# Kernel tuning notes

Hardware: AMD Instinct MI355X
Metric: run time of the kernel (lower is better)

## Reference

```python
import jax, jax.numpy as jnp
import numpy as np

D_MODEL, D_STATE, D_CONV, EXPAND = 1024, 16, 4, 2
D_INNER = D_MODEL * EXPAND
B, T = 1, 2048
EPS = 1e-5


def setup_inputs() -> dict:
    key = jax.random.key(0)
    ks = jax.random.split(key, 8)
    x = jax.random.normal(ks[0], (B, T, D_MODEL), dtype=jnp.float32)
    W_in = jax.random.normal(ks[1], (D_MODEL, 2 * D_INNER), dtype=jnp.float32) * 0.02
    conv_w = jax.random.normal(ks[2], (D_INNER, D_CONV), dtype=jnp.float32) * 0.2
    conv_b = jax.random.normal(ks[3], (D_INNER,), dtype=jnp.float32) * 0.02
    W_x = jax.random.normal(ks[4], (D_INNER, 2 * D_STATE + 1), dtype=jnp.float32) * 0.02
    W_dt = jax.random.normal(ks[5], (1, D_INNER), dtype=jnp.float32) * 0.5
    b_dt = jax.random.uniform(ks[6], (D_INNER,), dtype=jnp.float32, minval=-0.001, maxval=0.001)
    A_log = jnp.broadcast_to(jnp.log(jnp.arange(1, D_STATE + 1, dtype=jnp.float32))[None, :], (D_INNER, D_STATE))
    Dparam = jnp.ones((D_INNER,), dtype=jnp.float32)
    W_out = jax.random.normal(ks[7], (D_INNER, D_MODEL), dtype=jnp.float32) * 0.02
    ln_g = jnp.ones((D_MODEL,), dtype=jnp.float32)
    ln_b = jnp.zeros((D_MODEL,), dtype=jnp.float32)
    return {"x": x, "W_in": W_in, "conv_w": conv_w, "conv_b": conv_b, "W_x": W_x,
            "W_dt": W_dt, "b_dt": b_dt, "A_log": A_log, "D": Dparam,
            "W_out": W_out, "ln_g": ln_g, "ln_b": ln_b}


def _silu(v):
    return v * jax.nn.sigmoid(v)


def _layernorm(v, g, b):
    mu = jnp.mean(v, axis=-1, keepdims=True)
    var = jnp.mean((v - mu) ** 2, axis=-1, keepdims=True)
    return (v - mu) * jax.lax.rsqrt(var + EPS) * g + b


def _causal_depthwise_conv(xp, conv_w, conv_b):
    # xp: (B, T, D_INNER) -> (B, D_INNER, T) with left pad of D_CONV-1
    xc = jnp.swapaxes(xp, 1, 2)
    xc = jnp.pad(xc, ((0, 0), (0, 0), (D_CONV - 1, 0)))
    w = conv_w[:, None, :]  # (O=D_INNER, I/groups=1, K)
    out = jax.lax.conv_general_dilated(
        xc, w, window_strides=(1,), padding='VALID',
        dimension_numbers=('NCH', 'OIH', 'NCH'), feature_group_count=D_INNER)
    return jnp.swapaxes(out + conv_b[None, :, None], 1, 2)  # (B, T, D_INNER)


def reference(x, W_in, conv_w, conv_b, W_x, W_dt, b_dt, A_log, D, W_out, ln_g, ln_b):
    residual = x
    xn = _layernorm(x, ln_g, ln_b)
    xz = xn @ W_in                      # (B, T, 2*D_INNER)
    x_proj, z = jnp.split(xz, 2, axis=-1)
    x_conv = _silu(_causal_depthwise_conv(x_proj, conv_w, conv_b))  # (B, T, D_INNER)

    ssm = x_conv @ W_x                  # (B, T, 1 + 2*D_STATE)
    dt_raw = ssm[..., :1]
    Bp = ssm[..., 1:1 + D_STATE]        # (B, T, D_STATE)
    Cp = ssm[..., 1 + D_STATE:]         # (B, T, D_STATE)
    dt = jax.nn.softplus(dt_raw @ W_dt + b_dt)  # (B, T, D_INNER)

    A = -jnp.exp(A_log)                 # (D_INNER, D_STATE)
    A_bar = jnp.exp(dt[..., None] * A)                              # (B,T,d,n)
    Bx = dt[..., None] * Bp[:, :, None, :] * x_conv[..., None]      # (B,T,d,n)

    def step(h, inp):
        Ab_t, Bx_t, C_t = inp           # (B,d,n),(B,d,n),(B,n)
        h = Ab_t * h + Bx_t
        y_t = jnp.einsum('bdn,bn->bd', h, C_t)
        return h, y_t

    h0 = jnp.zeros((x.shape[0], D_INNER, D_STATE), dtype=x.dtype)
    _, ys = jax.lax.scan(step, h0, (jnp.swapaxes(A_bar, 0, 1),
                                    jnp.swapaxes(Bx, 0, 1),
                                    jnp.swapaxes(Cp, 0, 1)))
    y = jnp.swapaxes(ys, 0, 1)          # (B, T, D_INNER)

    y = y + x_conv * D
    y = y * _silu(z)
    return y @ W_out + residual
```

## Files before the change

kernel.cpp:

```cpp
#include <hip/hip_runtime.h>
#include <hip/hip_bf16.h>

typedef __hip_bfloat16 bf16;
typedef __attribute__((ext_vector_type(8))) short bf16x8;
typedef __attribute__((ext_vector_type(4))) float f32x4;
typedef __attribute__((ext_vector_type(2))) float f32x2;

#define T_LEN 2048
#define DMODEL 1024
#define DINNER 2048
#define DSTATE 16
#define LN_EPS 1e-5f
#define NCHUNK 128
#define CLEN 16
#define SSTR 64
#define PSEG 131072

#define GLOBAL_AS __attribute__((address_space(1)))
#define LDS_AS __attribute__((address_space(3)))

__device__ __forceinline__ void g2l16(void* lds, const void* g) {
    __builtin_amdgcn_global_load_lds((const GLOBAL_AS void*)g, (LDS_AS void*)lds, 16, 0, 0);
}

__device__ __forceinline__ float b2f(short s) {
    return __uint_as_float(((unsigned)(unsigned short)s) << 16);
}

__device__ __forceinline__ unsigned short f2bu(float f) {
    bf16 b = __float2bfloat16(f);
    return *reinterpret_cast<unsigned short*>(&b);
}

#define BG(buf, j) (buf[(j) >> 2][(j) & 3])

__global__ void prep_all(const float* __restrict__ Win, const float* __restrict__ Wout,
                         const float* __restrict__ Wx, const float* __restrict__ x,
                         const float* __restrict__ lng, const float* __restrict__ lnb,
                         bf16* __restrict__ WinT, bf16* __restrict__ WoutT,
                         bf16* __restrict__ WxT, bf16* __restrict__ xn) {
    __shared__ float t[32][33];
    int bid = blockIdx.x, tid = threadIdx.x;
    int tx = tid & 31, ty4 = (tid >> 5) * 4;
    if (bid < 4096) {
        int n0 = (bid & 127) * 32, k0 = (bid >> 7) * 32;
#pragma unroll
        for (int r = 0; r < 4; r++)
            t[ty4 + r][tx] = Win[(size_t)(k0 + ty4 + r) * 4096 + n0 + tx];
        __syncthreads();
#pragma unroll
        for (int r = 0; r < 4; r++)
            WinT[(size_t)(n0 + ty4 + r) * 1024 + k0 + tx] = __float2bfloat16(t[tx][ty4 + r]);
    } else if (bid < 6144) {
        int b = bid - 4096;
        int n0 = (b & 31) * 32, k0 = (b >> 5) * 32;
#pragma unroll
        for (int r = 0; r < 4; r++)
            t[ty4 + r][tx] = Wout[(size_t)(k0 + ty4 + r) * 1024 + n0 + tx];
        __syncthreads();
#pragma unroll
        for (int r = 0; r < 4; r++)
            WoutT[(size_t)(n0 + ty4 + r) * 2048 + k0 + tx] = __float2bfloat16(t[tx][ty4 + r]);
    } else if (bid < 6656) {
        int idx = (bid - 6144) * 256 + tid;
        int n = idx >> 11, k = idx & 2047;
        int j = (n == 0) ? 0 : (n >= 4 && n <= 35) ? n - 3 : -1;
        WxT[idx] = __float2bfloat16(j >= 0 ? Wx[k * 33 + j] : 0.f);
    } else {
        int row = bid - 6656;
        const float* xr = x + (size_t)row * DMODEL;
        float v[4];
        float s = 0.f, q = 0.f;
#pragma unroll
        for (int i = 0; i < 4; i++) {
            v[i] = xr[tid + i * 256];
            s += v[i];
            q += v[i] * v[i];
        }
        __shared__ float sh_s[256], sh_q[256];
        sh_s[tid] = s; sh_q[tid] = q;
        __syncthreads();
        for (int st = 128; st > 0; st >>= 1) {
            if (tid < st) { sh_s[tid] += sh_s[tid + st]; sh_q[tid] += sh_q[tid + st]; }
            __syncthreads();
        }
        float mean = sh_s[0] * (1.f / DMODEL);
        float var  = sh_q[0] * (1.f / DMODEL) - mean * mean;
        float rstd = rsqrtf(var + LN_EPS);
#pragma unroll
        for (int i = 0; i < 4; i++) {
            int c = tid + i * 256;
            xn[(size_t)row * DMODEL + c] =
                __float2bfloat16((v[i] - mean) * rstd * lng[c] + lnb[c]);
        }
    }
}

template <int BM, int BN, int WAVE_M, int WAVE_N, int WRITE_RESID, int OUT_BF16>
__global__ void gemm_mfma(const bf16* __restrict__ A, const bf16* __restrict__ Bt,
                          void* __restrict__ Cv, const float* __restrict__ resid,
                          int M, int N, int Kslice, int lda) {
    constexpr int WMsz = BM / WAVE_M;
    constexpr int WNsz = BN / WAVE_N;
    constexpr int TM = WMsz / 16;
    constexpr int TN = WNsz / 16;
    __shared__ short As[BM * 64];
    __shared__ short Bs[BN * 64];
    int tid = threadIdx.x;
    int lane = tid & 63, wave = tid >> 6;
    int wm = (wave / WAVE_N) * WMsz, wn = (wave % WAVE_N) * WNsz;
    int rowBase = blockIdx.y * BM, colBase = blockIdx.x * BN;
    int kbase = blockIdx.z * Kslice;

    f32x4 acc[TM][TN];
#pragma unroll
    for (int i = 0; i < TM; i++)
#pragma unroll
        for (int j = 0; j < TN; j++) acc[i][j] = f32x4{0.f, 0.f, 0.f, 0.f};

    int srow = tid >> 3;
    int cc = (tid & 7) ^ (srow & 7);
    const int ldsoff = tid * 16;

    for (int k0 = kbase; k0 < kbase + Kslice; k0 += 64) {
#pragma unroll
        for (int j = 0; j < BM / 32; j++)
            g2l16((char*)As + j * 4096 + ldsoff,
                  A + (size_t)(rowBase + j * 32 + srow) * lda + k0 + cc * 8);
#pragma unroll
        for (int j = 0; j < BN / 32; j++)
            g2l16((char*)Bs + j * 4096 + ldsoff,
                  Bt + (size_t)(colBase + j * 32 + srow) * lda + k0 + cc * 8);
        __syncthreads();
#pragma unroll
        for (int ks = 0; ks < 2; ks++) {
            bf16x8 af[TM], bfr[TN];
#pragma unroll
            for (int i = 0; i < TM; i++) {
                int row = wm + i * 16 + (lane & 15);
                int slot = (ks * 4 + (lane >> 4)) ^ (row & 7);
                af[i] = *(const bf16x8*)((const char*)As + row * 128 + slot * 16);
            }
#pragma unroll
            for (int j = 0; j < TN; j++) {
                int row = wn + j * 16 + (lane & 15);
                int slot = (ks * 4 + (lane >> 4)) ^ (row & 7);
                bfr[j] = *(const bf16x8*)((const char*)Bs + row * 128 + slot * 16);
            }
#pragma unroll
            for (int i = 0; i < TM; i++)
#pragma unroll
                for (int j = 0; j < TN; j++)
                    acc[i][j] = __builtin_amdgcn_mfma_f32_16x16x32_bf16(
                        af[i], bfr[j], acc[i][j], 0, 0, 0);
        }
        __syncthreads();
    }
    int rq = lane >> 4, cn = lane & 15;
    float* Cf = (float*)Cv + (size_t)blockIdx.z * M * N;
#pragma unroll
    for (int i = 0; i < TM; i++) {
#pragma unroll
        for (int j = 0; j < TN; j++) {
#pragma unroll
            for (int r = 0; r < 4; r++) {
                size_t row = rowBase + wm + i * 16 + rq * 4 + r;
                int col = colBase + wn + j * 16 + cn;
                float v = acc[i][j][r];
                if (WRITE_RESID) v += resid[row * N + col];
                if (OUT_BF16)
                    ((bf16*)Cv)[row * N + col] = __float2bfloat16(v);
                else
                    Cf[row * N + col] = v;
            }
        }
    }
}

__global__ void conv_silu(const bf16* __restrict__ xz, const float* __restrict__ cw,
                          const float* __restrict__ cb, bf16* __restrict__ xc) {
    int idx = blockIdx.x * 256 + threadIdx.x;
    int t = idx >> 9, d4 = (idx & 511) * 4;
    const f32x4 bv = *(const f32x4*)(cb + d4);
    float acc0 = bv[0], acc1 = bv[1], acc2 = bv[2], acc3 = bv[3];
    const f32x4* cwv = (const f32x4*)(cw + d4 * 4);
    f32x4 w0 = cwv[0], w1 = cwv[1], w2 = cwv[2], w3 = cwv[3];
#pragma unroll
    for (int k = 0; k < 4; k++) {
        int tt = t - 3 + k;
        if (tt >= 0) {
            ushort4 v = *(const ushort4*)((const short*)xz + (size_t)tt * (2 * DINNER) + d4);
            acc0 = fmaf(b2f((short)v.x), w0[k], acc0);
            acc1 = fmaf(b2f((short)v.y), w1[k], acc1);
            acc2 = fmaf(b2f((short)v.z), w2[k], acc2);
            acc3 = fmaf(b2f((short)v.w), w3[k], acc3);
        }
    }
    ushort4 o;
    o.x = f2bu(acc0 / (1.f + __expf(-acc0)));
    o.y = f2bu(acc1 / (1.f + __expf(-acc1)));
    o.z = f2bu(acc2 / (1.f + __expf(-acc2)));
    o.w = f2bu(acc3 / (1.f + __expf(-acc3)));
    *(ushort4*)((short*)xc + (size_t)t * DINNER + d4) = o;
}

__global__ void reduce_parts(const float* __restrict__ parts, float* __restrict__ ssm) {
    int idx = (blockIdx.x * 256 + threadIdx.x) * 4;
    f32x4 a = *(const f32x4*)(parts + idx);
    f32x4 b = *(const f32x4*)(parts + idx + PSEG);
    f32x4 c = *(const f32x4*)(parts + idx + 2 * PSEG);
    f32x4 d = *(const f32x4*)(parts + idx + 3 * PSEG);
    *(f32x4*)(ssm + idx) = (a + b) + (c + d);
}

__device__ __forceinline__ float softplus_f(float pre) {
    return (pre > 20.f) ? pre : log1pf(__expf(pre));
}

__device__ __forceinline__ void powtree(float q, float* a) {
    a[0] = q;
    a[1] = q * q;
    a[2] = a[1] * q;
    a[3] = a[1] * a[1];
#pragma unroll
    for (int j = 0; j < 4; j++) a[4 + j] = a[j] * a[3];
#pragma unroll
    for (int j = 0; j < 8; j++) a[8 + j] = a[j] * a[7];
}

__device__ __forceinline__ void ldrow5(f32x4* b, const f32x4* sp) {
#pragma unroll
    for (int k = 0; k < 5; k++) b[k] = sp[k];
}

__device__ __forceinline__ void ldrow8(f32x4* b, const f32x4* sp) {
#pragma unroll
    for (int k = 0; k < 8; k++) b[k] = sp[k];
}

template <int FAST>
__device__ __forceinline__ void p1_step(const f32x4* buf, short xcs, float wdt, float bd,
                                        const float* A, float& Lsum, float* Sv,
                                        f32x2* dqout) {
    float dt = softplus_f(BG(buf, 0) * wdt + bd);
    float q = __expf(-dt);
    Lsum += dt;
    float u = dt * b2f(xcs);
    *dqout = f32x2{dt, q};
    if (FAST) {
        float a[DSTATE];
        powtree(q, a);
#pragma unroll
        for (int n = 0; n < DSTATE; n++)
            Sv[n] = fmaf(a[n], Sv[n], u * BG(buf, 4 + n));
    } else {
#pragma unroll
        for (int n = 0; n < DSTATE; n++)
            Sv[n] = fmaf(__expf(dt * A[n]), Sv[n], u * BG(buf, 4 + n));
    }
}

template <int FAST>
__device__ __forceinline__ void p1_loop(const f32x4* sp, const short* xcp,
                                        float wdt, float bd, const float* A,
                                        float& Lsum, float* Sv, f32x2* dqp) {
    short xcv[CLEN];
#pragma unroll
    for (int i = 0; i < CLEN; i++)
        xcv[i] = xcp[(size_t)i * DINNER];
    f32x4 bA[5], bB[5];
    ldrow5(bA, sp);
#pragma unroll
    for (int i = 0; i < CLEN; i += 2) {
        ldrow5(bB, sp + (i + 1) * 16);
        p1_step<FAST>(bA, xcv[i], wdt, bd, A, Lsum, Sv, dqp + (size_t)i * DINNER);
        ldrow5(bA, sp + (i + 2) * 16);
        p1_step<FAST>(bB, xcv[i + 1], wdt, bd, A, Lsum, Sv, dqp + (size_t)(i + 1) * DINNER);
    }
}

__global__ void scan_pass1(
        const float* __restrict__ ssm, const bf16* __restrict__ xc,
        const float* __restrict__ Wdt, const float* __restrict__ bdt,
        const float* __restrict__ Alog,
        float* __restrict__ Ld, float* __restrict__ S, f32x2* __restrict__ dq) {
    int tid = threadIdx.x;
    int d = blockIdx.x * 256 + tid;
    int c = blockIdx.y;
    int t0 = c * CLEN;
    float A[DSTATE];
    bool fast = true;
#pragma unroll
    for (int n = 0; n < DSTATE; n++) {
        A[n] = -__expf(Alog[d * DSTATE + n]);
        fast = fast && (fabsf(A[n] + (float)(n + 1)) < 1e-3f * (n + 1));
    }
    float wdt = Wdt[d], bd = bdt[d];
    float Sv[DSTATE];
#pragma unroll
    for (int n = 0; n < DSTATE; n++) Sv[n] = 0.f;
    float Lsum = 0.f;
    const f32x4* sp = (const f32x4*)(ssm + (size_t)t0 * SSTR);
    const short* xcp = (const short*)xc + (size_t)t0 * DINNER + d;
    f32x2* dqp = dq + (size_t)t0 * DINNER + d;
    if (fast)
        p1_loop<1>(sp, xcp, wdt, bd, A, Lsum, Sv, dqp);
    else
        p1_loop<0>(sp, xcp, wdt, bd, A, Lsum, Sv, dqp);
    Ld[(size_t)c * DINNER + d] = Lsum;
    size_t base = (size_t)c * DINNER * DSTATE + d;
#pragma unroll
    for (int n = 0; n < DSTATE; n++)
        S[base + (size_t)n * DINNER] = Sv[n];
}

#define SEGL (NCHUNK / 4)
__global__ void scan_pass2(const float* __restrict__ Ld, const float* __restrict__ S,
                           const float* __restrict__ Alog, float* __restrict__ Hst) {
    int tx = threadIdx.x & 63, ty = threadIdx.x >> 6;
    int d = blockIdx.x * 64 + tx;
    int n = blockIdx.y;
    float A = -__expf(Alog[d * DSTATE + n]);
    int c0 = ty * SEGL;
    float lv[SEGL], sv[SEGL];
#pragma unroll
    for (int j = 0; j < SEGL; j++) {
        int cc = c0 + j;
        lv[j] = Ld[(size_t)cc * DINNER + d];
        sv[j] = S[(size_t)cc * DINNER * DSTATE + (size_t)n * DINNER + d];
    }
    float Lsum = 0.f, Sseg = 0.f;
#pragma unroll
    for (int j = 0; j < SEGL; j++) {
        Sseg = fmaf(__expf(A * lv[j]), Sseg, sv[j]);
        Lsum += lv[j];
    }
    __shared__ float shL[4][64], shS[4][64], shC[4][64];
    shL[ty][tx] = Lsum;
    shS[ty][tx] = Sseg;
    __syncthreads();
    if (ty == 0) {
        float car = 0.f;
        shC[0][tx] = 0.f;
#pragma unroll
        for (int s = 0; s < 3; s++) {
            car = fmaf(__expf(A * shL[s][tx]), car, shS[s][tx]);
            shC[s + 1][tx] = car;
        }
    }
    __syncthreads();
    float H = shC[ty][tx];
#pragma unroll
    for (int j = 0; j < SEGL; j++) {
        size_t o = (size_t)(c0 + j) * DINNER * DSTATE + (size_t)n * DINNER + d;
        Hst[o] = H;
        H = fmaf(__expf(A * lv[j]), H, sv[j]);
    }
}

template <int FAST>
__device__ __forceinline__ void p3_step(const f32x4* buf, f32x2 dq, short xcs, short zs,
                                        float Dd, const float* A,
                                        float* h, bf16* outp) {
    float dt = dq[0], q = dq[1];
    float xcf = b2f(xcs);
    float u = dt * xcf;
    float y;
    if (FAST) {
        float a[DSTATE];
        powtree(q, a);
        float y0 = 0.f, y1 = 0.f, y2 = 0.f, y3 = 0.f;
#pragma unroll
        for (int n = 0; n < 4; n++) {
            h[n]      = fmaf(a[n],      h[n],      u * BG(buf, n));
            y0 = fmaf(h[n],      BG(buf, 16 + n), y0);
            h[n + 4]  = fmaf(a[n + 4],  h[n + 4],  u * BG(buf, 4 + n));
            y1 = fmaf(h[n + 4],  BG(buf, 20 + n), y1);
            h[n + 8]  = fmaf(a[n + 8],  h[n + 8],  u * BG(buf, 8 + n));
            y2 = fmaf(h[n + 8],  BG(buf, 24 + n), y2);
            h[n + 12] = fmaf(a[n + 12], h[n + 12], u * BG(buf, 12 + n));
            y3 = fmaf(h[n + 12], BG(buf, 28 + n), y3);
        }
        y = (y0 + y1) + (y2 + y3);
    } else {
        y = 0.f;
#pragma unroll
        for (int n = 0; n < DSTATE; n++) {
            float a = __expf(dt * A[n]);
            h[n] = fmaf(a, h[n], u * BG(buf, n));
            y = fmaf(h[n], BG(buf, 16 + n), y);
        }
    }
    float z = b2f(zs);
    float sz = z / (1.f + __expf(-z));
    *outp = __float2bfloat16(fmaf(xcf, Dd, y) * sz);
}

template <int FAST>
__device__ __forceinline__ void p3_loop(const f32x4* sp8, const f32x2* dqp,
                                        const short* xcp, const short* zp,
                                        float Dd, const float* A,
                                        float* h, bf16* yp) {
    f32x2 dqv[CLEN];
    short xcv[CLEN], zv[CLEN];
#pragma unroll
    for (int i = 0; i < CLEN; i++) {
        dqv[i] = dqp[(size_t)i * DINNER];
        xcv[i] = xcp[(size_t)i * DINNER];
        zv[i]  = zp[(size_t)i * 2 * DINNER];
    }
    f32x4 bA[8], bB[8];
    ldrow8(bA, sp8);
#pragma unroll
    for (int i = 0; i < CLEN; i += 2) {
        ldrow8(bB, sp8 + (i + 1) * 16);
        p3_step<FAST>(bA, dqv[i], xcv[i], zv[i], Dd, A, h, yp + (size_t)i * DINNER);
        ldrow8(bA, sp8 + (i + 2) * 16);
        p3_step<FAST>(bB, dqv[i + 1], xcv[i + 1], zv[i + 1], Dd, A, h,
                      yp + (size_t)(i + 1) * DINNER);
    }
}

__global__ void scan_pass3(
        const float* __restrict__ ssm, const f32x2* __restrict__ dq,
        const bf16* __restrict__ xc, const bf16* __restrict__ xz,
        const float* __restrict__ Alog, const float* __restrict__ Dp,
        const float* __restrict__ Hst, bf16* __restrict__ yf) {
    int tid = threadIdx.x;
    int d = blockIdx.x * 256 + tid;
    int c = blockIdx.y;
    int t0 = c * CLEN;
    float A[DSTATE], h[DSTATE];
    bool fast = true;
    size_t base = (size_t)c * DINNER * DSTATE + d;
#pragma unroll
    for (int n = 0; n < DSTATE; n++) {
        A[n] = -__expf(Alog[d * DSTATE + n]);
        fast = fast && (fabsf(A[n] + (float)(n + 1)) < 1e-3f * (n + 1));
        h[n] = Hst[base + (size_t)n * DINNER];
    }
    float Dd = Dp[d];
    const f32x4* sp8 = (const f32x4*)(ssm + (size_t)t0 * SSTR) + 1;
    const f32x2* dqp = dq + (size_t)t0 * DINNER + d;
    const short* xcp = (const short*)xc + (size_t)t0 * DINNER + d;
    const short* zp  = (const short*)xz + (size_t)t0 * (2 * DINNER) + DINNER + d;
    bf16* yp = yf + (size_t)t0 * DINNER + d;
    if (fast)
        p3_loop<1>(sp8, dqp, xcp, zp, Dd, A, h, yp);
    else
        p3_loop<0>(sp8, dqp, xcp, zp, Dd, A, h, yp);
}

extern "C" void kernel_launch(void* const* d_in, const int* in_sizes, int n_in,
                              void* d_out, int out_size, void* d_ws, size_t ws_size,
                              hipStream_t stream) {
    const float* x     = (const float*)d_in[0];
    const float* W_in  = (const float*)d_in[1];
    const float* convw = (const float*)d_in[2];
    const float* convb = (const float*)d_in[3];
    const float* W_x   = (const float*)d_in[4];
    const float* W_dt  = (const float*)d_in[5];
    const float* b_dt  = (const float*)d_in[6];
    const float* A_log = (const float*)d_in[7];
    const float* Dp    = (const float*)d_in[8];
    const float* W_out = (const float*)d_in[9];
    const float* ln_g  = (const float*)d_in[10];
    const float* ln_b  = (const float*)d_in[11];
    float* out = (float*)d_out;

    char* wsb = (char*)d_ws;
    bf16*  xn    = (bf16*)(wsb);
    bf16*  WinT  = (bf16*)(wsb + (4ull  << 20));
    bf16*  WoutT = (bf16*)(wsb + (12ull << 20));
    bf16*  WxT   = (bf16*)(wsb + (16ull << 20));
    bf16*  xz    = (bf16*)(wsb + (17ull << 20));
    bf16*  xc    = (bf16*)(wsb + (33ull << 20));
    float* parts = (float*)(wsb + (41ull << 20));
    float* Ld    = (float*)(wsb + (43ull << 20));
    float* Hst   = (float*)(wsb + (44ull << 20));
    float* S     = (float*)(wsb + (60ull << 20));
    bf16*  yf    = (bf16*)(wsb + (76ull << 20));
    float* ssm   = (float*)(wsb + (84ull << 20));
    f32x2* dq    = (f32x2*)(wsb + (86ull << 20));

    prep_all<<<8704, 256, 0, stream>>>(W_in, W_out, W_x, x, ln_g, ln_b,
                                       WinT, WoutT, WxT, xn);

    gemm_mfma<128, 128, 2, 2, 0, 1><<<dim3(4096 / 128, 2048 / 128), 256, 0, stream>>>(
        xn, WinT, xz, nullptr, 2048, 4096, 1024, 1024);

    conv_silu<<<(T_LEN * DINNER / 4) / 256, 256, 0, stream>>>(xz, convw, convb, xc);

    gemm_mfma<32, 64, 2, 2, 0, 0><<<dim3(1, 2048 / 32, 4), 256, 0, stream>>>(
        xc, WxT, parts, nullptr, 2048, 64, 512, 2048);

    reduce_parts<<<(T_LEN * SSTR / 4) / 256, 256, 0, stream>>>(parts, ssm);

    scan_pass1<<<dim3(DINNER / 256, NCHUNK), 256, 0, stream>>>(
        ssm, xc, W_dt, b_dt, A_log, Ld, S, dq);
    scan_pass2<<<dim3(DINNER / 64, DSTATE), 256, 0, stream>>>(Ld, S, A_log, Hst);
    scan_pass3<<<dim3(DINNER / 256, NCHUNK), 256, 0, stream>>>(
        ssm, dq, xc, xz, A_log, Dp, Hst, yf);

    gemm_mfma<64, 64, 2, 2, 1, 0><<<dim3(1024 / 64, 2048 / 64), 256, 0, stream>>>(
        yf, WoutT, out, x, 2048, 1024, 2048, 2048);
}
```

Baseline: 221.2 us.

## Fuse three scan passes into one cooperative kernel with grid syncs

Merges scan_pass1/2/3 into a single cooperative kernel with 1024 blocks that keeps dt, xc and z values in registers across two grid.sync barriers, so the dq intermediate is never written or reread and two launches go away. The x_proj GEMM also moves from a 4-way to an 8-way K split to expose more parallelism, and the reduce kernel grows to match. If the cooperative launch fails, the old three-kernel path runs as a fallback. Risks are grid.sync overhead, the occupancy limit imposed by launch_bounds, and the extra partial-sum traffic from the wider K split.

```diff
diff --git a/kernel.cpp b/kernel.cpp
--- a/kernel.cpp
+++ b/kernel.cpp
@@ -1,5 +1,8 @@
 #include <hip/hip_runtime.h>
 #include <hip/hip_bf16.h>
+#include <hip/hip_cooperative_groups.h>
+
+namespace cg = cooperative_groups;
 
 typedef __hip_bfloat16 bf16;
 typedef __attribute__((ext_vector_type(8))) short bf16x8;
@@ -15,6 +18,7 @@
 #define CLEN 16
 #define SSTR 64
 #define PSEG 131072
+#define KSPLIT 8
 
 #define GLOBAL_AS __attribute__((address_space(1)))
 #define LDS_AS __attribute__((address_space(3)))
@@ -206,11 +210,11 @@
 
 __global__ void reduce_parts(const float* __restrict__ parts, float* __restrict__ ssm) {
     int idx = (blockIdx.x * 256 + threadIdx.x) * 4;
-    f32x4 a = *(const f32x4*)(parts + idx);
-    f32x4 b = *(const f32x4*)(parts + idx + PSEG);
-    f32x4 c = *(const f32x4*)(parts + idx + 2 * PSEG);
-    f32x4 d = *(const f32x4*)(parts + idx + 3 * PSEG);
-    *(f32x4*)(ssm + idx) = (a + b) + (c + d);
+    f32x4 s = f32x4{0.f, 0.f, 0.f, 0.f};
+#pragma unroll
+    for (int k = 0; k < KSPLIT; k++)
+        s += *(const f32x4*)(parts + idx + (size_t)k * PSEG);
+    *(f32x4*)(ssm + idx) = s;
 }
 
 __device__ __forceinline__ float softplus_f(float pre) {
@@ -239,17 +243,16 @@
 }
 
 template <int FAST>
-__device__ __forceinline__ void p1_step(const f32x4* buf, short xcs, float wdt, float bd,
-                                        const float* A, float& Lsum, float* Sv,
-                                        f32x2* dqout) {
+__device__ __forceinline__ void pf1_step(const f32x4* buf, short xcs, float wdt, float bd,
+                                         const float* A, float& Lsum, float* Sv,
+                                         float& dtout) {
     float dt = softplus_f(BG(buf, 0) * wdt + bd);
-    float q = __expf(-dt);
+    dtout = dt;
     Lsum += dt;
     float u = dt * b2f(xcs);
-    *dqout = f32x2{dt, q};
     if (FAST) {
         float a[DSTATE];
-        powtree(q, a);
+        powtree(__expf(-dt), a);
 #pragma unroll
         for (int n = 0; n < DSTATE; n++)
             Sv[n] = fmaf(a[n], Sv[n], u * BG(buf, 4 + n));
@@ -261,21 +264,180 @@
 }
 
 template <int FAST>
-__device__ __forceinline__ void p1_loop(const f32x4* sp, const short* xcp,
-                                        float wdt, float bd, const float* A,
-                                        float& Lsum, float* Sv, f32x2* dqp) {
-    short xcv[CLEN];
-#pragma unroll
-    for (int i = 0; i < CLEN; i++)
+__device__ __forceinline__ void pf3_step(const f32x4* buf, float dt, short xcs, short zs,
+                                         float Dd, const float* A,
+                                         float* h, bf16* outp) {
+    float xcf = b2f(xcs);
+    float u = dt * xcf;
+    float y;
+    if (FAST) {
+        float a[DSTATE];
+        powtree(__expf(-dt), a);
+        float y0 = 0.f, y1 = 0.f, y2 = 0.f, y3 = 0.f;
+#pragma unroll
+        for (int n = 0; n < 4; n++) {
+            h[n]      = fmaf(a[n],      h[n],      u * BG(buf, n));
+            y0 = fmaf(h[n],      BG(buf, 16 + n), y0);
+            h[n + 4]  = fmaf(a[n + 4],  h[n + 4],  u * BG(buf, 4 + n));
+            y1 = fmaf(h[n + 4],  BG(buf, 20 + n), y1);
+            h[n + 8]  = fmaf(a[n + 8],  h[n + 8],  u * BG(buf, 8 + n));
+            y2 = fmaf(h[n + 8],  BG(buf, 24 + n), y2);
+            h[n + 12] = fmaf(a[n + 12], h[n + 12], u * BG(buf, 12 + n));
+            y3 = fmaf(h[n + 12], BG(buf, 28 + n), y3);
+        }
+        y = (y0 + y1) + (y2 + y3);
+    } else {
+        y = 0.f;
+#pragma unroll
+        for (int n = 0; n < DSTATE; n++) {
+            float a = __expf(dt * A[n]);
+            h[n] = fmaf(a, h[n], u * BG(buf, n));
+            y = fmaf(h[n], BG(buf, 16 + n), y);
+        }
+    }
+    float z = b2f(zs);
+    float sz = z / (1.f + __expf(-z));
+    *outp = __float2bfloat16(fmaf(xcf, Dd, y) * sz);
+}
+
+#define SEGL (NCHUNK / 4)
+__global__ __launch_bounds__(256, 4) void scan_fused(
+        const float* __restrict__ ssm, const bf16* __restrict__ xc,
+        const bf16* __restrict__ xz,
+        const float* __restrict__ Wdt, const float* __restrict__ bdt,
+        const float* __restrict__ Alog, const float* __restrict__ Dp,
+        float* __restrict__ Ld, float* __restrict__ S,
+        float* __restrict__ Hst, bf16* __restrict__ yf) {
+    cg::grid_group grid = cg::this_grid();
+    int tid = threadIdx.x;
+    int b = blockIdx.x;
+    int dg = b & 7, c = b >> 3;
+    int d = dg * 256 + tid;
+    int t0 = c * CLEN;
+
+    float A[DSTATE];
+    bool fast = true;
+#pragma unroll
+    for (int n = 0; n < DSTATE; n++) {
+        A[n] = -__expf(Alog[d * DSTATE + n]);
+        fast = fast && (fabsf(A[n] + (float)(n + 1)) < 1e-3f * (n + 1));
+    }
+    float wdt = Wdt[d], bd = bdt[d];
+    const short* xcp = (const short*)xc + (size_t)t0 * DINNER + d;
+    const short* zp  = (const short*)xz + (size_t)t0 * (2 * DINNER) + DINNER + d;
+    short xcv[CLEN], zv[CLEN];
+#pragma unroll
+    for (int i = 0; i < CLEN; i++) {
         xcv[i] = xcp[(size_t)i * DINNER];
-    f32x4 bA[5], bB[5];
-    ldrow5(bA, sp);
-#pragma unroll
-    for (int i = 0; i < CLEN; i += 2) {
-        ldrow5(bB, sp + (i + 1) * 16);
-        p1_step<FAST>(bA, xcv[i], wdt, bd, A, Lsum, Sv, dqp + (size_t)i * DINNER);
-        ldrow5(bA, sp + (i + 2) * 16);
-        p1_step<FAST>(bB, xcv[i + 1], wdt, bd, A, Lsum, Sv, dqp + (size_t)(i + 1) * DINNER);
+        zv[i]  = zp[(size_t)i * 2 * DINNER];
+    }
+    float dtv[CLEN];
+    float Sv[DSTATE];
+#pragma unroll
+    for (int n = 0; n < DSTATE; n++) Sv[n] = 0.f;
+    float Lsum = 0.f;
+    const f32x4* sp = (const f32x4*)(ssm + (size_t)t0 * SSTR);
+    if (fast) {
+        f32x4 bA[5], bB[5];
+        ldrow5(bA, sp);
+#pragma unroll
+        for (int i = 0; i < CLEN; i += 2) {
+            ldrow5(bB, sp + (i + 1) * 16);
+            pf1_step<1>(bA, xcv[i], wdt, bd, A, Lsum, Sv, dtv[i]);
+            ldrow5(bA, sp + (i + 2) * 16);
+            pf1_step<1>(bB, xcv[i + 1], wdt, bd, A, Lsum, Sv, dtv[i + 1]);
+        }
+    } else {
+        f32x4 bA[5], bB[5];
+        ldrow5(bA, sp);
+#pragma unroll
+        for (int i = 0; i < CLEN; i += 2) {
+            ldrow5(bB, sp + (i + 1) * 16);
+            pf1_step<0>(bA, xcv[i], wdt, bd, A, Lsum, Sv, dtv[i]);
+            ldrow5(bA, sp + (i + 2) * 16);
+            pf1_step<0>(bB, xcv[i + 1], wdt, bd, A, Lsum, Sv, dtv[i + 1]);
+        }
+    }
+    Ld[(size_t)c * DINNER + d] = Lsum;
+    size_t base = (size_t)c * DINNER * DSTATE + d;
+#pragma unroll
+    for (int n = 0; n < DSTATE; n++)
+        S[base + (size_t)n * DINNER] = Sv[n];
+
+    grid.sync();
+
+    if (b < 512) {
+        int tx = tid & 63, ty = tid >> 6;
+        int d2 = (b & 31) * 64 + tx;
+        int n2 = b >> 5;
+        float A2 = -__expf(Alog[d2 * DSTATE + n2]);
+        int c0 = ty * SEGL;
+        float Lsum2 = 0.f, Sseg = 0.f;
+#pragma unroll 8
+        for (int j = 0; j < SEGL; j++) {
+            int cc = c0 + j;
+            float lv = Ld[(size_t)cc * DINNER + d2];
+            float sv = S[(size_t)cc * DINNER * DSTATE + (size_t)n2 * DINNER + d2];
+            Sseg = fmaf(__expf(A2 * lv), Sseg, sv);
+            Lsum2 += lv;
+        }
+        __shared__ float shL[4][64], shS[4][64], shC[4][64];
+        shL[ty][tx] = Lsum2;
+        shS[ty][tx] = Sseg;
+        __syncthreads();
+        if (ty == 0) {
+            float car = 0.f;
+            shC[0][tx] = 0.f;
+#pragma unroll
+            for (int s = 0; s < 3; s++) {
+                car = fmaf(__expf(A2 * shL[s][tx]), car, shS[s][tx]);
+                shC[s + 1][tx] = car;
+            }
+        }
+        __syncthreads();
+        float H = shC[ty][tx];
+#pragma unroll 8
+        for (int j = 0; j < SEGL; j++) {
+            int cc = c0 + j;
+            size_t o = (size_t)cc * DINNER * DSTATE + (size_t)n2 * DINNER + d2;
+            float sv = S[o];
+            float lv = Ld[(size_t)cc * DINNER + d2];
+            Hst[o] = H;
+            H = fmaf(__expf(A2 * lv), H, sv);
+        }
+    }
+
+    grid.sync();
+
+    float h[DSTATE];
+#pragma unroll
+    for (int n = 0; n < DSTATE; n++)
+        h[n] = Hst[base + (size_t)n * DINNER];
+    float Dd = Dp[d];
+    const f32x4* sp8 = sp + 1;
+    bf16* yp = yf + (size_t)t0 * DINNER + d;
+    if (fast) {
+        f32x4 bA[8], bB[8];
+        ldrow8(bA, sp8);
+#pragma unroll
+        for (int i = 0; i < CLEN; i += 2) {
+            ldrow8(bB, sp8 + (i + 1) * 16);
+            pf3_step<1>(bA, dtv[i], xcv[i], zv[i], Dd, A, h, yp + (size_t)i * DINNER);
+            ldrow8(bA, sp8 + (i + 2) * 16);
+            pf3_step<1>(bB, dtv[i + 1], xcv[i + 1], zv[i + 1], Dd, A, h,
+                        yp + (size_t)(i + 1) * DINNER);
+        }
+    } else {
+        f32x4 bA[8], bB[8];
+        ldrow8(bA, sp8);
+#pragma unroll
+        for (int i = 0; i < CLEN; i += 2) {
+            ldrow8(bB, sp8 + (i + 1) * 16);
+            pf3_step<0>(bA, dtv[i], xcv[i], zv[i], Dd, A, h, yp + (size_t)i * DINNER);
+            ldrow8(bA, sp8 + (i + 2) * 16);
+            pf3_step<0>(bB, dtv[i + 1], xcv[i + 1], zv[i + 1], Dd, A, h,
+                        yp + (size_t)(i + 1) * DINNER);
+        }
     }
 }
 
@@ -303,10 +465,35 @@
     const f32x4* sp = (const f32x4*)(ssm + (size_t)t0 * SSTR);
     const short* xcp = (const short*)xc + (size_t)t0 * DINNER + d;
     f32x2* dqp = dq + (size_t)t0 * DINNER + d;
-    if (fast)
-        p1_loop<1>(sp, xcp, wdt, bd, A, Lsum, Sv, dqp);
-    else
-        p1_loop<0>(sp, xcp, wdt, bd, A, Lsum, Sv, dqp);
+    short xcv[CLEN];
+#pragma unroll
+    for (int i = 0; i < CLEN; i++)
+        xcv[i] = xcp[(size_t)i * DINNER];
+    float dtv[CLEN];
+    if (fast) {
+        f32x4 bA[5], bB[5];
+        ldrow5(bA, sp);
+#pragma unroll
+        for (int i = 0; i < CLEN; i += 2) {
+            ldrow5(bB, sp + (i + 1) * 16);
+            pf1_step<1>(bA, xcv[i], wdt, bd, A, Lsum, Sv, dtv[i]);
+            ldrow5(bA, sp + (i + 2) * 16);
+            pf1_step<1>(bB, xcv[i + 1], wdt, bd, A, Lsum, Sv, dtv[i + 1]);
+        }
+    } else {
+        f32x4 bA[5], bB[5];
+        ldrow5(bA, sp);
+#pragma unroll
+        for (int i = 0; i < CLEN; i += 2) {
+            ldrow5(bB, sp + (i + 1) * 16);
+            pf1_step<0>(bA, xcv[i], wdt, bd, A, Lsum, Sv, dtv[i]);
+            ldrow5(bA, sp + (i + 2) * 16);
+            pf1_step<0>(bB, xcv[i + 1], wdt, bd, A, Lsum, Sv, dtv[i + 1]);
+        }
+    }
+#pragma unroll
+    for (int i = 0; i < CLEN; i++)
+        dqp[(size_t)i * DINNER] = f32x2{dtv[i], __expf(-dtv[i])};
     Ld[(size_t)c * DINNER + d] = Lsum;
     size_t base = (size_t)c * DINNER * DSTATE + d;
 #pragma unroll
@@ -314,7 +501,6 @@
         S[base + (size_t)n * DINNER] = Sv[n];
 }
 
-#define SEGL (NCHUNK / 4)
 __global__ void scan_pass2(const float* __restrict__ Ld, const float* __restrict__ S,
                            const float* __restrict__ Alog, float* __restrict__ Hst) {
     int tx = threadIdx.x & 63, ty = threadIdx.x >> 6;
@@ -355,69 +541,6 @@
         size_t o = (size_t)(c0 + j) * DINNER * DSTATE + (size_t)n * DINNER + d;
         Hst[o] = H;
         H = fmaf(__expf(A * lv[j]), H, sv[j]);
-    }
-}
-
-template <int FAST>
-__device__ __forceinline__ void p3_step(const f32x4* buf, f32x2 dq, short xcs, short zs,
-                                        float Dd, const float* A,
-                                        float* h, bf16* outp) {
-    float dt = dq[0], q = dq[1];
-    float xcf = b2f(xcs);
-    float u = dt * xcf;
-    float y;
-    if (FAST) {
-        float a[DSTATE];
-        powtree(q, a);
-        float y0 = 0.f, y1 = 0.f, y2 = 0.f, y3 = 0.f;
-#pragma unroll
-        for (int n = 0; n < 4; n++) {
-            h[n]      = fmaf(a[n],      h[n],      u * BG(buf, n));
-            y0 = fmaf(h[n],      BG(buf, 16 + n), y0);
-            h[n + 4]  = fmaf(a[n + 4],  h[n + 4],  u * BG(buf, 4 + n));
-            y1 = fmaf(h[n + 4],  BG(buf, 20 + n), y1);
-            h[n + 8]  = fmaf(a[n + 8],  h[n + 8],  u * BG(buf, 8 + n));
-            y2 = fmaf(h[n + 8],  BG(buf, 24 + n), y2);
-            h[n + 12] = fmaf(a[n + 12], h[n + 12], u * BG(buf, 12 + n));
-            y3 = fmaf(h[n + 12], BG(buf, 28 + n), y3);
-        }
-        y = (y0 + y1) + (y2 + y3);
-    } else {
-        y = 0.f;
-#pragma unroll
-        for (int n = 0; n < DSTATE; n++) {
-            float a = __expf(dt * A[n]);
-            h[n] = fmaf(a, h[n], u * BG(buf, n));
-            y = fmaf(h[n], BG(buf, 16 + n), y);
-        }
-    }
-    float z = b2f(zs);
-    float sz = z / (1.f + __expf(-z));
-    *outp = __float2bfloat16(fmaf(xcf, Dd, y) * sz);
-}
-
-template <int FAST>
-__device__ __forceinline__ void p3_loop(const f32x4* sp8, const f32x2* dqp,
-                                        const short* xcp, const short* zp,
-                                        float Dd, const float* A,
-                                        float* h, bf16* yp) {
-    f32x2 dqv[CLEN];
-    short xcv[CLEN], zv[CLEN];
-#pragma unroll
-    for (int i = 0; i < CLEN; i++) {
-        dqv[i] = dqp[(size_t)i * DINNER];
-        xcv[i] = xcp[(size_t)i * DINNER];
-        zv[i]  = zp[(size_t)i * 2 * DINNER];
-    }
-    f32x4 bA[8], bB[8];
-    ldrow8(bA, sp8);
-#pragma unroll
-    for (int i = 0; i < CLEN; i += 2) {
-        ldrow8(bB, sp8 + (i + 1) * 16);
-        p3_step<FAST>(bA, dqv[i], xcv[i], zv[i], Dd, A, h, yp + (size_t)i * DINNER);
-        ldrow8(bA, sp8 + (i + 2) * 16);
-        p3_step<FAST>(bB, dqv[i + 1], xcv[i + 1], zv[i + 1], Dd, A, h,
-                      yp + (size_t)(i + 1) * DINNER);
     }
 }
 
@@ -445,10 +568,37 @@
     const short* xcp = (const short*)xc + (size_t)t0 * DINNER + d;
     const short* zp  = (const short*)xz + (size_t)t0 * (2 * DINNER) + DINNER + d;
     bf16* yp = yf + (size_t)t0 * DINNER + d;
-    if (fast)
-        p3_loop<1>(sp8, dqp, xcp, zp, Dd, A, h, yp);
-    else
-        p3_loop<0>(sp8, dqp, xcp, zp, Dd, A, h, yp);
+    f32x2 dqv[CLEN];
+    short xcv[CLEN], zv[CLEN];
+#pragma unroll
+    for (int i = 0; i < CLEN; i++) {
+        dqv[i] = dqp[(size_t)i * DINNER];
+        xcv[i] = xcp[(size_t)i * DINNER];
+        zv[i]  = zp[(size_t)i * 2 * DINNER];
+    }
+    if (fast) {
+        f32x4 bA[8], bB[8];
+        ldrow8(bA, sp8);
+#pragma unroll
+        for (int i = 0; i < CLEN; i += 2) {
+            ldrow8(bB, sp8 + (i + 1) * 16);
+            pf3_step<1>(bA, dqv[i][0], xcv[i], zv[i], Dd, A, h, yp + (size_t)i * DINNER);
+            ldrow8(bA, sp8 + (i + 2) * 16);
+            pf3_step<1>(bB, dqv[i + 1][0], xcv[i + 1], zv[i + 1], Dd, A, h,
+                        yp + (size_t)(i + 1) * DINNER);
+        }
+    } else {
+        f32x4 bA[8], bB[8];
+        ldrow8(bA, sp8);
+#pragma unroll
+        for (int i = 0; i < CLEN; i += 2) {
+            ldrow8(bB, sp8 + (i + 1) * 16);
+            pf3_step<0>(bA, dqv[i][0], xcv[i], zv[i], Dd, A, h, yp + (size_t)i * DINNER);
+            ldrow8(bA, sp8 + (i + 2) * 16);
+            pf3_step<0>(bB, dqv[i + 1][0], xcv[i + 1], zv[i + 1], Dd, A, h,
+                        yp + (size_t)(i + 1) * DINNER);
+        }
+    }
 }
 
 extern "C" void kernel_launch(void* const* d_in, const int* in_sizes, int n_in,
@@ -476,12 +626,12 @@
     bf16*  xz    = (bf16*)(wsb + (17ull << 20));
     bf16*  xc    = (bf16*)(wsb + (33ull << 20));
     float* parts = (float*)(wsb + (41ull << 20));
-    float* Ld    = (float*)(wsb + (43ull << 20));
-    float* Hst   = (float*)(wsb + (44ull << 20));
-    float* S     = (float*)(wsb + (60ull << 20));
-    bf16*  yf    = (bf16*)(wsb + (76ull << 20));
-    float* ssm   = (float*)(wsb + (84ull << 20));
-    f32x2* dq    = (f32x2*)(wsb + (86ull << 20));
+    float* Ld    = (float*)(wsb + (45ull << 20));
+    float* Hst   = (float*)(wsb + (46ull << 20));
+    float* S     = (float*)(wsb + (62ull << 20));
+    bf16*  yf    = (bf16*)(wsb + (78ull << 20));
+    float* ssm   = (float*)(wsb + (86ull << 20));
+    f32x2* dq    = (f32x2*)(wsb + (88ull << 20));
 
     prep_all<<<8704, 256, 0, stream>>>(W_in, W_out, W_x, x, ln_g, ln_b,
                                        WinT, WoutT, WxT, xn);
@@ -491,16 +641,24 @@
 
     conv_silu<<<(T_LEN * DINNER / 4) / 256, 256, 0, stream>>>(xz, convw, convb, xc);
 
-    gemm_mfma<32, 64, 2, 2, 0, 0><<<dim3(1, 2048 / 32, 4), 256, 0, stream>>>(
-        xc, WxT, parts, nullptr, 2048, 64, 512, 2048);
+    gemm_mfma<32, 64, 2, 2, 0, 0><<<dim3(1, 2048 / 32, KSPLIT), 256, 0, stream>>>(
+        xc, WxT, parts, nullptr, 2048, 64, 2048 / KSPLIT, 2048);
 
     reduce_parts<<<(T_LEN * SSTR / 4) / 256, 256, 0, stream>>>(parts, ssm);
 
-    scan_pass1<<<dim3(DINNER / 256, NCHUNK), 256, 0, stream>>>(
-        ssm, xc, W_dt, b_dt, A_log, Ld, S, dq);
-    scan_pass2<<<dim3(DINNER / 64, DSTATE), 256, 0, stream>>>(Ld, S, A_log, Hst);
-    scan_pass3<<<dim3(DINNER / 256, NCHUNK), 256, 0, stream>>>(
-        ssm, dq, xc, xz, A_log, Dp, Hst, yf);
+    void* kargs[] = {(void*)&ssm, (void*)&xc, (void*)&xz, (void*)&W_dt, (void*)&b_dt,
+                     (void*)&A_log, (void*)&Dp, (void*)&Ld, (void*)&S, (void*)&Hst,
+                     (void*)&yf};
+    hipError_t cerr = hipLaunchCooperativeKernel((void*)scan_fused, dim3(1024),
+                                                 dim3(256), kargs, 0, stream);
+    if (cerr != hipSuccess) {
+        (void)hipGetLastError();
+        scan_pass1<<<dim3(DINNER / 256, NCHUNK), 256, 0, stream>>>(
+            ssm, xc, W_dt, b_dt, A_log, Ld, S, dq);
+        scan_pass2<<<dim3(DINNER / 64, DSTATE), 256, 0, stream>>>(Ld, S, A_log, Hst);
+        scan_pass3<<<dim3(DINNER / 256, NCHUNK), 256, 0, stream>>>(
+            ssm, dq, xc, xz, A_log, Dp, Hst, yf);
+    }
 
     gemm_mfma<64, 64, 2, 2, 1, 0><<<dim3(1024 / 64, 2048 / 64), 256, 0, stream>>>(
         yf, WoutT, out, x, 2048, 1024, 2048, 2048);
```

Result: slower. 460.6 us (+108.2%).
